# Optimization experiments

Measured on AMD Instinct MI355X. Metric: run time of the kernel, lower is better.

Reference implementation:

```python
import jax, jax.numpy as jnp
import numpy as np


def setup_inputs() -> dict:
    key = jax.random.key(0)
    k1, k2 = jax.random.split(key)
    T, J, d = 16384, 64, 1024
    h = jax.random.normal(k1, (1, T, d), dtype=jnp.float32)
    s = jax.random.normal(k2, (T, J), dtype=jnp.float32)
    return {"h": h, "s": s}


def reference(h, s):
    # z1 = max over query axis, b = softmax over context positions  [T]
    b = jax.nn.softmax(jnp.max(s, axis=-1))
    # weighted sum of context vectors: sum_t b[t] * h[0, t, :]  -> [d]
    ctx = jnp.einsum('t,td->d', b, h[0])
    # tile the attended vector across all T positions -> [d, T]
    T = s.shape[0]
    q2c = jnp.broadcast_to(ctx[:, None], (ctx.shape[0], T))
    return q2c
```

## Files before the change

### kernel.cpp

```cpp
#include <hip/hip_runtime.h>
#include <math.h>

#define T_DIM 16384
#define J_DIM 64
#define D_DIM 1024

#define NB   512
#define RPB  32

#define MB_OFF   0
#define ZB_OFF   512
#define PART_OFF 1024

__global__ __launch_bounds__(256) void kb_heavy(const float* __restrict__ h,
                                                const float* __restrict__ s,
                                                float* __restrict__ ws) {
    __shared__ float rowmax[RPB];
    __shared__ float wts[RPB];
    const int tid = threadIdx.x;
    const int b = blockIdx.x;

    const float4* s4 = (const float4*)s + (size_t)b * (RPB * J_DIM / 4);
    float4 v0 = s4[tid];
    float4 v1 = s4[tid + 256];
    float m0 = fmaxf(fmaxf(v0.x, v0.y), fmaxf(v0.z, v0.w));
    float m1 = fmaxf(fmaxf(v1.x, v1.y), fmaxf(v1.z, v1.w));
#pragma unroll
    for (int off = 1; off < 16; off <<= 1) {
        m0 = fmaxf(m0, __shfl_xor(m0, off));
        m1 = fmaxf(m1, __shfl_xor(m1, off));
    }
    if ((tid & 15) == 0) {
        rowmax[tid >> 4] = m0;
        rowmax[16 + (tid >> 4)] = m1;
    }
    __syncthreads();

    if (tid == 0) {
        float Mb = rowmax[0];
#pragma unroll
        for (int r = 1; r < RPB; ++r) Mb = fmaxf(Mb, rowmax[r]);
        float Zb = 0.f;
#pragma unroll
        for (int r = 0; r < RPB; ++r) {
            const float w = expf(rowmax[r] - Mb);
            wts[r] = w;
            Zb += w;
        }
        ws[MB_OFF + b] = Mb;
        ws[ZB_OFF + b] = Zb;
    }
    __syncthreads();

    const float4* h4 = (const float4*)h;
    float4 acc = make_float4(0.f, 0.f, 0.f, 0.f);
    const size_t base = (size_t)b * (RPB * D_DIM / 4) + tid;
#pragma unroll 8
    for (int r = 0; r < RPB; ++r) {
        const float4 v = h4[base + (size_t)r * (D_DIM / 4)];
        const float wt = wts[r];
        acc.x = fmaf(wt, v.x, acc.x);
        acc.y = fmaf(wt, v.y, acc.y);
        acc.z = fmaf(wt, v.z, acc.z);
        acc.w = fmaf(wt, v.w, acc.w);
    }

    ((float4*)(ws + PART_OFF))[(size_t)b * (D_DIM / 4) + tid] = acc;
}

__global__ __launch_bounds__(256) void kcd_reduce_bcast(const float* __restrict__ ws,
                                                        float4* __restrict__ out4) {
    __shared__ float redm[256];
    __shared__ float redz[256];
    __shared__ float redc[256];
    const int tid = threadIdx.x;
    const int dd = blockIdx.x;

    const float m0 = ws[MB_OFF + tid];
    const float m1 = ws[MB_OFF + tid + 256];
    const float* prow = ws + PART_OFF + (size_t)tid * D_DIM + dd;
    const float p0 = prow[0];
    const float p1 = prow[(size_t)256 * D_DIM];
    const float z0 = ws[ZB_OFF + tid];
    const float z1 = ws[ZB_OFF + tid + 256];

    redm[tid] = fmaxf(m0, m1);
    __syncthreads();
#pragma unroll
    for (int off = 128; off > 0; off >>= 1) {
        if (tid < off) redm[tid] = fmaxf(redm[tid], redm[tid + off]);
        __syncthreads();
    }
    const float M = redm[0];

    const float s0 = expf(m0 - M);
    const float s1 = expf(m1 - M);
    redz[tid] = s0 * z0 + s1 * z1;
    redc[tid] = s0 * p0 + s1 * p1;
    __syncthreads();
#pragma unroll
    for (int off = 128; off > 0; off >>= 1) {
        if (tid < off) {
            redz[tid] += redz[tid + off];
            redc[tid] += redc[tid + off];
        }
        __syncthreads();
    }
    const float val = redc[0] / redz[0];

    const float4 v4 = make_float4(val, val, val, val);
    float4* o = out4 + (size_t)dd * (T_DIM / 4);
#pragma unroll
    for (int i = 0; i < T_DIM / 4 / 256; ++i)
        o[(size_t)i * 256 + tid] = v4;
}

extern "C" void kernel_launch(void* const* d_in, const int* in_sizes, int n_in,
                              void* d_out, int out_size, void* d_ws, size_t ws_size,
                              hipStream_t stream) {
    const float* h = (const float*)d_in[0];
    const float* s = (const float*)d_in[1];
    float* ws = (float*)d_ws;
    float4* out = (float4*)d_out;

    kb_heavy<<<NB, 256, 0, stream>>>(h, s, ws);
    kcd_reduce_bcast<<<D_DIM, 256, 0, stream>>>(ws, out);
}
```

Before: 116.2 us.

## Fuse partial-sum and reduce/broadcast kernels into one cooperative grid-synced kernel

Merges the two launches into one cooperative kernel with 512 blocks, separated by grid-wide syncs. The output buffer stands in for the workspace: partial sums are staged there, then a second grid sync guards the overwrite with the final broadcast. Each block reduces two output columns instead of one and writes the broadcast with nontemporal stores. This removes a kernel launch boundary and the workspace traffic, at the cost of two grid barriers and a co-residency requirement for all 512 blocks.

```diff
diff --git a/kernel.cpp b/kernel.cpp
--- a/kernel.cpp
+++ b/kernel.cpp
@@ -1,5 +1,8 @@
 #include <hip/hip_runtime.h>
+#include <hip/hip_cooperative_groups.h>
 #include <math.h>
+
+namespace cg = cooperative_groups;
 
 #define T_DIM 16384
 #define J_DIM 64
@@ -8,17 +11,24 @@
 #define NB   512
 #define RPB  32
 
-#define MB_OFF   0
-#define ZB_OFF   512
-#define PART_OFF 1024
+#define PART_OFF 0
+#define MB_OFF   (NB * D_DIM)
+#define ZB_OFF   (MB_OFF + NB)
 
-__global__ __launch_bounds__(256) void kb_heavy(const float* __restrict__ h,
-                                                const float* __restrict__ s,
-                                                float* __restrict__ ws) {
+typedef float floatx4 __attribute__((ext_vector_type(4)));
+
+__global__ __launch_bounds__(256) void fused(const float* __restrict__ h,
+                                             const float* __restrict__ s,
+                                             float* __restrict__ out) {
     __shared__ float rowmax[RPB];
     __shared__ float wts[RPB];
+    __shared__ float redm[256];
+    __shared__ float redz[256];
+    __shared__ float redc0[256];
+    __shared__ float redc1[256];
+
     const int tid = threadIdx.x;
-    const int b = blockIdx.x;
+    const int b   = blockIdx.x;
 
     const float4* s4 = (const float4*)s + (size_t)b * (RPB * J_DIM / 4);
     float4 v0 = s4[tid];
@@ -47,8 +57,8 @@
             wts[r] = w;
             Zb += w;
         }
-        ws[MB_OFF + b] = Mb;
-        ws[ZB_OFF + b] = Zb;
+        out[MB_OFF + b] = Mb;
+        out[ZB_OFF + b] = Zb;
     }
     __syncthreads();
 
@@ -64,27 +74,23 @@
         acc.z = fmaf(wt, v.z, acc.z);
         acc.w = fmaf(wt, v.w, acc.w);
     }
+    ((float4*)(out + PART_OFF))[(size_t)b * (D_DIM / 4) + tid] = acc;
 
-    ((float4*)(ws + PART_OFF))[(size_t)b * (D_DIM / 4) + tid] = acc;
-}
+    cg::this_grid().sync();
 
-__global__ __launch_bounds__(256) void kcd_reduce_bcast(const float* __restrict__ ws,
-                                                        float4* __restrict__ out4) {
-    __shared__ float redm[256];
-    __shared__ float redz[256];
-    __shared__ float redc[256];
-    const int tid = threadIdx.x;
-    const int dd = blockIdx.x;
+    const int dd0 = 2 * b;
+    const int dd1 = 2 * b + 1;
+    const float bm0 = out[MB_OFF + tid];
+    const float bm1 = out[MB_OFF + tid + 256];
+    const float* prow = out + PART_OFF + (size_t)tid * D_DIM;
+    const float p00 = prow[dd0];
+    const float p01 = prow[dd1];
+    const float p10 = prow[(size_t)256 * D_DIM + dd0];
+    const float p11 = prow[(size_t)256 * D_DIM + dd1];
+    const float bz0 = out[ZB_OFF + tid];
+    const float bz1 = out[ZB_OFF + tid + 256];
 
-    const float m0 = ws[MB_OFF + tid];
-    const float m1 = ws[MB_OFF + tid + 256];
-    const float* prow = ws + PART_OFF + (size_t)tid * D_DIM + dd;
-    const float p0 = prow[0];
-    const float p1 = prow[(size_t)256 * D_DIM];
-    const float z0 = ws[ZB_OFF + tid];
-    const float z1 = ws[ZB_OFF + tid + 256];
-
-    redm[tid] = fmaxf(m0, m1);
+    redm[tid] = fmaxf(bm0, bm1);
     __syncthreads();
 #pragma unroll
     for (int off = 128; off > 0; off >>= 1) {
@@ -93,26 +99,35 @@
     }
     const float M = redm[0];
 
-    const float s0 = expf(m0 - M);
-    const float s1 = expf(m1 - M);
-    redz[tid] = s0 * z0 + s1 * z1;
-    redc[tid] = s0 * p0 + s1 * p1;
+    const float sc0 = expf(bm0 - M);
+    const float sc1 = expf(bm1 - M);
+    redz[tid]  = sc0 * bz0 + sc1 * bz1;
+    redc0[tid] = sc0 * p00 + sc1 * p10;
+    redc1[tid] = sc0 * p01 + sc1 * p11;
     __syncthreads();
 #pragma unroll
     for (int off = 128; off > 0; off >>= 1) {
         if (tid < off) {
-            redz[tid] += redz[tid + off];
-            redc[tid] += redc[tid + off];
+            redz[tid]  += redz[tid + off];
+            redc0[tid] += redc0[tid + off];
+            redc1[tid] += redc1[tid + off];
         }
         __syncthreads();
     }
-    const float val = redc[0] / redz[0];
+    const float val0 = redc0[0] / redz[0];
+    const float val1 = redc1[0] / redz[0];
 
-    const float4 v4 = make_float4(val, val, val, val);
-    float4* o = out4 + (size_t)dd * (T_DIM / 4);
+    cg::this_grid().sync();
+
+    const floatx4 w0 = { val0, val0, val0, val0 };
+    const floatx4 w1 = { val1, val1, val1, val1 };
+    floatx4* o0 = (floatx4*)out + (size_t)dd0 * (T_DIM / 4);
+    floatx4* o1 = (floatx4*)out + (size_t)dd1 * (T_DIM / 4);
 #pragma unroll
-    for (int i = 0; i < T_DIM / 4 / 256; ++i)
-        o[(size_t)i * 256 + tid] = v4;
+    for (int i = 0; i < T_DIM / 4 / 256; ++i) {
+        __builtin_nontemporal_store(w0, o0 + (size_t)i * 256 + tid);
+        __builtin_nontemporal_store(w1, o1 + (size_t)i * 256 + tid);
+    }
 }
 
 extern "C" void kernel_launch(void* const* d_in, const int* in_sizes, int n_in,
@@ -120,9 +135,8 @@
                               hipStream_t stream) {
     const float* h = (const float*)d_in[0];
     const float* s = (const float*)d_in[1];
-    float* ws = (float*)d_ws;
-    float4* out = (float4*)d_out;
-
-    kb_heavy<<<NB, 256, 0, stream>>>(h, s, ws);
-    kcd_reduce_bcast<<<D_DIM, 256, 0, stream>>>(ws, out);
+    float* out = (float*)d_out;
+    void* args[] = { (void*)&h, (void*)&s, (void*)&out };
+    (void)hipLaunchCooperativeKernel((const void*)fused, dim3(NB), dim3(256),
+                                     args, 0, stream);
 }
```

Result: slower. 249.1 us (+114.3%).
